# Performance work log

Measured on AMD Instinct MI355X. Metric: run time of the kernel, lower is better.

The kernel has to match this reference:

```python
import jax, jax.numpy as jnp
import numpy as np

N_NODES = 20000   # len(pert2id)
N_EDGES = 400000  # top_20 graph: ~20 edges/node
BATCH   = 4096
IN_DIM  = 64
HID_DIM = 128
OUT_DIM = 64
HEADS   = 2
HEAD_D  = HID_DIM // HEADS  # 64 (also OUT_DIM per head on last layer)


def setup_inputs() -> dict:
    key = jax.random.key(0)
    ks = jax.random.split(key, 24)
    inp = {
        "pert_indices": jax.random.randint(ks[0], (BATCH,), 0, N_NODES),
        "edge_index": jax.random.randint(ks[1], (2, N_EDGES), 0, N_NODES),
        "edge_weight": jax.random.uniform(ks[2], (N_EDGES,), dtype=jnp.float32),
        "emb": jax.random.normal(ks[3], (N_NODES, IN_DIM), dtype=jnp.float32) * 0.02,
    }
    # 4 GATv2 layers: layer0 IN->HEADS*HEAD_D (concat), layers 1,2 HID->HEADS*HEAD_D (concat),
    # layer3 HID->HEADS*OUT_DIM (mean over heads -> OUT_DIM)
    in_dims = [IN_DIM, HID_DIM, HID_DIM, HID_DIM]
    concat = [True, True, True, False]
    k = 4
    for i in range(4):
        d_in = in_dims[i]
        d_head = HEAD_D
        sc = 1.0 / np.sqrt(d_in)
        inp[f"Wl{i}"] = jax.random.normal(ks[k], (d_in, HEADS * d_head), dtype=jnp.float32) * sc; k += 1
        inp[f"Wr{i}"] = jax.random.normal(ks[k], (d_in, HEADS * d_head), dtype=jnp.float32) * sc; k += 1
        inp[f"a{i}"]  = jax.random.normal(ks[k], (HEADS, d_head), dtype=jnp.float32) * (1.0 / np.sqrt(d_head)); k += 1
        out_dim = HEADS * d_head if concat[i] else d_head
        inp[f"b{i}"]  = jnp.zeros((out_dim,), dtype=jnp.float32); k += 1
    return inp


def _gatv2_layer(x, src, dst, ew, Wl, Wr, a, b, concat):
    N = x.shape[0]
    H, D = a.shape
    xl = (x @ Wl).reshape(N, H, D)   # source transform (messages)
    xr = (x @ Wr).reshape(N, H, D)   # target transform
    # GATv2 score: a^T LeakyReLU(Wl x_j + Wr x_i) per edge, per head -> [E, H]
    e = jnp.einsum("ehd,hd->eh", jax.nn.leaky_relu(xl[src] + xr[dst], 0.2), a)
    # segment softmax over incoming edges of each target node
    m = jax.ops.segment_max(e, dst, num_segments=N)
    m = jnp.where(jnp.isfinite(m), m, 0.0)  # isolated nodes
    ex = jnp.exp(e - m[dst])
    s = jax.ops.segment_sum(ex, dst, num_segments=N)
    alpha = ex / (s[dst] + 1e-16)            # [E, H]
    msg = (alpha * ew[:, None])[:, :, None] * xl[src]  # edge-weighted messages [E,H,D]
    out = jax.ops.segment_sum(msg, dst, num_segments=N)  # [N,H,D]
    out = out.reshape(N, H * D) if concat else out.mean(axis=1)
    return out + b


def reference(pert_indices, edge_index, edge_weight, emb,
              Wl0, Wr0, a0, b0, Wl1, Wr1, a1, b1,
              Wl2, Wr2, a2, b2, Wl3, Wr3, a3, b3):
    src, dst = edge_index[0], edge_index[1]
    layers = [(Wl0, Wr0, a0, b0, True), (Wl1, Wr1, a1, b1, True),
              (Wl2, Wr2, a2, b2, True), (Wl3, Wr3, a3, b3, False)]
    x = emb
    for i, (Wl, Wr, a, b, cc) in enumerate(layers):
        x = _gatv2_layer(x, src, dst, edge_weight, Wl, Wr, a, b, cc)
        if i < len(layers) - 1:
            x = jax.nn.elu(x)
    # node_emb[pert_indices]
    return x[pert_indices]
```

## Files before the change

### kernel.cpp

```cpp
#include <hip/hip_runtime.h>
#include <hip/hip_fp16.h>
#include <math.h>

#define N_NODES 20000
#define N_EDGES 400000
#define BATCH   4096
#define MTILES  (N_NODES / 16)
#define XSCALE  1024.0f
#define XINV    (1.0f / 1024.0f)

typedef __attribute__((ext_vector_type(8))) short short8v;
typedef __attribute__((ext_vector_type(4))) float f32x4;

__device__ __forceinline__ void bf16split(float v, short& h, short& l)
{
    unsigned u  = __float_as_uint(v);
    unsigned hu = u & 0xFFFF0000u;
    h = (short)(hu >> 16);
    const float lo = v - __uint_as_float(hu);
    l = (short)(__float_as_uint(lo) >> 16);
}

__global__ __launch_bounds__(256)
void pack_w_all_kernel(const float* __restrict__ Wl0, const float* __restrict__ Wr0,
                       const float* __restrict__ Wl1, const float* __restrict__ Wr1,
                       const float* __restrict__ Wl2, const float* __restrict__ Wr2,
                       const float* __restrict__ Wl3, const float* __restrict__ Wr3,
                       short* __restrict__ wpk)
{
    const int t = blockIdx.x * 256 + threadIdx.x;
    if (t >= 14336) return;
    int layer, base, K;
    const float *Wl, *Wr;
    if (t < 2048)       { layer = 0; base = 0;     K = 64;  Wl = Wl0; Wr = Wr0; }
    else if (t < 6144)  { layer = 1; base = 2048;  K = 128; Wl = Wl1; Wr = Wr1; }
    else if (t < 10240) { layer = 2; base = 6144;  K = 128; Wl = Wl2; Wr = Wr2; }
    else                { layer = 3; base = 10240; K = 128; Wl = Wl3; Wr = Wr3; }
    const int KB   = K / 32;
    const int tt   = t - base;
    const int lane = tt & 63;
    const int kb   = (tt >> 6) % KB;
    const int nt   = tt / (64 * KB);
    const float* W = (nt < 8) ? Wl : Wr;
    const int col  = (nt & 7) * 16 + (lane & 15);
    const int k0   = kb * 32 + (lane >> 4) * 8;
    short8v h, l;
#pragma unroll
    for (int e = 0; e < 8; ++e) {
        short hh, ll; bf16split(W[(size_t)(k0 + e) * 128 + col], hh, ll);
        h[e] = hh; l[e] = ll;
    }
    short* ob = wpk + (size_t)layer * 65536
                    + ((size_t)(nt * KB + kb) * 2) * 512 + lane * 8;
    *(short8v*)ob         = h;
    *(short8v*)(ob + 512) = l;
}

template<int KB, int NWAVES>
__global__ __launch_bounds__(NWAVES * 64)
void mfma_transform_kernel(const float* __restrict__ x,
                           const short* __restrict__ wpk,
                           __half* __restrict__ xlh, float* __restrict__ xr)
{
    constexpr int K  = KB * 32;
    constexpr int KP = K + 4;
    __shared__ float xs[16 * KP];
    const int mtile = blockIdx.x;
    const int wid   = threadIdx.x >> 6;
    const int lane  = threadIdx.x & 63;

    {
        const float4* __restrict__ src = (const float4*)(x + (size_t)mtile * 16 * K);
        for (int idx = threadIdx.x; idx < 16 * K / 4; idx += NWAVES * 64) {
            const int row = idx / (K / 4), c4 = idx % (K / 4);
            *(float4*)(xs + row * KP + c4 * 4) = src[idx];
        }
    }
    __syncthreads();

    short8v ah[KB], al[KB];
    {
        const float* ab = xs + (lane & 15) * KP + (lane >> 4) * 8;
#pragma unroll
        for (int kb = 0; kb < KB; ++kb) {
            const float4 f0 = *(const float4*)(ab + kb * 32);
            const float4 f1 = *(const float4*)(ab + kb * 32 + 4);
            float tmp[8] = {f0.x, f0.y, f0.z, f0.w, f1.x, f1.y, f1.z, f1.w};
#pragma unroll
            for (int e = 0; e < 8; ++e) {
                short hh, ll; bf16split(tmp[e], hh, ll);
                ah[kb][e] = hh; al[kb][e] = ll;
            }
        }
    }

#pragma unroll
    for (int i = 0; i < 4; ++i) {
        const int nt = wid * 4 + i;
        const short* bb = wpk + ((size_t)nt * KB * 2) * 512 + lane * 8;
        f32x4 acc = {0.f, 0.f, 0.f, 0.f};
#pragma unroll
        for (int kb = 0; kb < KB; ++kb) {
            const short8v bh = *(const short8v*)(bb + (size_t)(kb * 2 + 0) * 512);
            const short8v bl = *(const short8v*)(bb + (size_t)(kb * 2 + 1) * 512);
            acc = __builtin_amdgcn_mfma_f32_16x16x32_bf16(ah[kb], bh, acc, 0, 0, 0);
            acc = __builtin_amdgcn_mfma_f32_16x16x32_bf16(ah[kb], bl, acc, 0, 0, 0);
            acc = __builtin_amdgcn_mfma_f32_16x16x32_bf16(al[kb], bh, acc, 0, 0, 0);
        }
        const int colb = (nt & 7) * 16 + (lane & 15);
        const int row0 = mtile * 16 + (lane >> 4) * 4;
        if (nt < 8) {
#pragma unroll
            for (int r = 0; r < 4; ++r)
                xlh[(size_t)(row0 + r) * 128 + colb] = __float2half(acc[r] * XSCALE);
        } else {
#pragma unroll
            for (int r = 0; r < 4; ++r)
                xr[(size_t)(row0 + r) * 128 + colb] = acc[r];
        }
    }
}

template<int K, int G>
__global__ __launch_bounds__(128)
void transform_r_pert_kernel(const float* __restrict__ x,
                             const int* __restrict__ pert,
                             const float* __restrict__ W,
                             float* __restrict__ out)
{
    const int t  = threadIdx.x;
    const int i0 = blockIdx.x * G;

    const float* __restrict__ xrow[G];
#pragma unroll
    for (int g = 0; g < G; ++g)
        xrow[g] = x + (size_t)pert[i0 + g] * K;

    float acc[G];
#pragma unroll
    for (int g = 0; g < G; ++g) acc[g] = 0.f;

    float4 xA[G], xB[G];
    float wA[4], wB[4];

    auto loadc = [&](float4* xs, float* w, int k) {
#pragma unroll
        for (int g = 0; g < G; ++g)
            xs[g] = *(const float4*)(xrow[g] + k);
#pragma unroll
        for (int u = 0; u < 4; ++u) w[u] = W[(k + u) * 128 + t];
    };
    auto fmac = [&](const float4* xs, const float* w) {
#pragma unroll
        for (int g = 0; g < G; ++g) {
            acc[g] = fmaf(xs[g].x, w[0], acc[g]);
            acc[g] = fmaf(xs[g].y, w[1], acc[g]);
            acc[g] = fmaf(xs[g].z, w[2], acc[g]);
            acc[g] = fmaf(xs[g].w, w[3], acc[g]);
        }
    };

    loadc(xA, wA, 0);
    for (int k0 = 0; k0 < K; k0 += 8) {
        if (k0 + 4 < K) loadc(xB, wB, k0 + 4);
        fmac(xA, wA);
        if (k0 + 8 < K) loadc(xA, wA, k0 + 8);
        fmac(xB, wB);
    }

#pragma unroll
    for (int g = 0; g < G; ++g)
        out[(size_t)(i0 + g) * 128 + t] = acc[g];
}

__global__ __launch_bounds__(256)
void zero_kernel(int* __restrict__ p, int n)
{
    const int i = blockIdx.x * blockDim.x + threadIdx.x;
    if (i < n) p[i] = 0;
}

__global__ __launch_bounds__(256)
void count_deg_kernel(const int* __restrict__ dst, int* __restrict__ deg, int E)
{
    const int e = blockIdx.x * blockDim.x + threadIdx.x;
    if (e < E) atomicAdd(&deg[dst[e]], 1);
}

#define CHUNK 20
#define SCAN_PAD (1024 * CHUNK)
__global__ __launch_bounds__(1024)
void scan_kernel(const int* __restrict__ deg, int* __restrict__ off,
                 int* __restrict__ cursor)
{
    __shared__ int xs[SCAN_PAD];
    __shared__ int sums[1024];
    const int t = threadIdx.x;
    for (int i = t; i < SCAN_PAD; i += 1024)
        xs[i] = (i < N_NODES) ? deg[i] : 0;
    __syncthreads();

    const int base = t * CHUNK;
    int local[CHUNK];
    int s = 0;
#pragma unroll
    for (int i = 0; i < CHUNK; ++i) {
        local[i] = s;
        s += xs[base + i];
    }
    sums[t] = s;
    __syncthreads();
    for (int d = 1; d < 1024; d <<= 1) {
        int v = (t >= d) ? sums[t - d] : 0;
        __syncthreads();
        sums[t] += v;
        __syncthreads();
    }
    const int prev = (t == 0) ? 0 : sums[t - 1];
#pragma unroll
    for (int i = 0; i < CHUNK; ++i)
        xs[base + i] = prev + local[i];
    __syncthreads();
    for (int i = t; i < N_NODES; i += 1024) {
        const int o = xs[i];
        off[i] = o;
        cursor[i] = o;
    }
    if (t == 1023) off[N_NODES] = sums[1023];
}

__global__ __launch_bounds__(256)
void scatter_kernel(const int* __restrict__ src, const int* __restrict__ dst,
                    const float* __restrict__ ew, int* __restrict__ cursor,
                    int* __restrict__ ssrc, float* __restrict__ sew, int E)
{
    const int e = blockIdx.x * blockDim.x + threadIdx.x;
    if (e >= E) return;
    const int p = atomicAdd(&cursor[dst[e]], 1);
    ssrc[p] = src[e];
    sew[p]  = ew[e];
}

template<int LAST>
__global__ __launch_bounds__(256)
void gat_node_kernel(const __half* __restrict__ xl, const float* __restrict__ xr,
                     const int* __restrict__ off, const int* __restrict__ ssrc,
                     const float* __restrict__ sew, const float* __restrict__ a,
                     const float* __restrict__ b, float* __restrict__ xout,
                     const int* __restrict__ nodemap, int nnodes)
{
    const int widx = (int)((blockIdx.x * blockDim.x + threadIdx.x) >> 6);
    if (widx >= nnodes) return;
    const int node = LAST ? nodemap[widx] : widx;
    const int xrrow = widx;
    const int lane = threadIdx.x & 63;
    const int q  = lane >> 4;
    const int h  = (lane >> 3) & 1;
    const int j  = lane & 7;
    const int cb = h * 64 + j * 8;

    const float* xrp = xr + (size_t)xrrow * 128 + cb;
    const float4 rA = make_float4(xrp[0] * XSCALE, xrp[1] * XSCALE,
                                  xrp[2] * XSCALE, xrp[3] * XSCALE);
    const float4 rB = make_float4(xrp[4] * XSCALE, xrp[5] * XSCALE,
                                  xrp[6] * XSCALE, xrp[7] * XSCALE);
    const float4 aA = *(const float4*)(a + cb);
    const float4 aB = *(const float4*)(a + cb + 4);

    const int e0 = off[node], e1 = off[node + 1];
    const int nr = (e1 - e0 + 3) >> 2;

    float m = -1e30f, s = 0.f;
    float4 accA = {0,0,0,0}, accB = {0,0,0,0};

    auto ldh8 = [](const __half* p, float4& lo, float4& hi) {
        const uint4 raw = *(const uint4*)p;
        const float2 f0 = __half22float2(*(const __half2*)&raw.x);
        const float2 f1 = __half22float2(*(const __half2*)&raw.y);
        const float2 f2 = __half22float2(*(const __half2*)&raw.z);
        const float2 f3 = __half22float2(*(const __half2*)&raw.w);
        lo = make_float4(f0.x, f0.y, f1.x, f1.y);
        hi = make_float4(f2.x, f2.y, f3.x, f3.y);
    };
    auto lrelu4 = [](float4 v) {
        v.x = fmaxf(v.x, 0.2f * v.x); v.y = fmaxf(v.y, 0.2f * v.y);
        v.z = fmaxf(v.z, 0.2f * v.z); v.w = fmaxf(v.w, 0.2f * v.w);
        return v;
    };
    auto dot4 = [](float4 u, float4 v) {
        return fmaf(u.x, v.x, fmaf(u.y, v.y, fmaf(u.z, v.z, u.w * v.w)));
    };
    auto upd4 = [](float4 acc, float r, float c, float4 xv) {
        acc.x = fmaf(c, xv.x, acc.x * r); acc.y = fmaf(c, xv.y, acc.y * r);
        acc.z = fmaf(c, xv.z, acc.z * r); acc.w = fmaf(c, xv.w, acc.w * r);
        return acc;
    };
    auto lde = [&](int r, float& w, bool& valid, float4& xA, float4& xB) {
        const int ei  = e0 + r * 4 + q;
        valid = ei < e1;
        const int eic = valid ? ei : (e1 - 1);
        const int sn  = ssrc[eic];
        w = valid ? sew[eic] : 0.f;
        ldh8(xl + (size_t)sn * 128 + cb, xA, xB);
    };

    float w_c; bool v_c; float4 xA_c, xB_c;
    if (nr > 0) lde(0, w_c, v_c, xA_c, xB_c);

    for (int r = 0; r < nr; ++r) {
        float w_n; bool v_n; float4 xA_n, xB_n;
        if (r + 1 < nr) lde(r + 1, w_n, v_n, xA_n, xB_n);

        const float4 vA = lrelu4(make_float4(xA_c.x + rA.x, xA_c.y + rA.y,
                                             xA_c.z + rA.z, xA_c.w + rA.w));
        const float4 vB = lrelu4(make_float4(xB_c.x + rB.x, xB_c.y + rB.y,
                                             xB_c.z + rB.z, xB_c.w + rB.w));
        float p = dot4(vA, aA) + dot4(vB, aB);
        p += __shfl_xor(p, 1, 64);
        p += __shfl_xor(p, 2, 64);
        p += __shfl_xor(p, 4, 64);
        p = v_c ? p * XINV : -1e30f;

        const float d   = p - m;
        const float t   = __expf(-fabsf(d));
        const bool  pos = d > 0.f;
        const float rr  = pos ? t : 1.f;
        const float ex  = pos ? 1.f : t;
        m = pos ? p : m;
        const float c = ex * w_c;
        s = s * rr + ex;
        accA = upd4(accA, rr, c, xA_c);
        accB = upd4(accB, rr, c, xB_c);

        w_c = w_n; v_c = v_n; xA_c = xA_n; xB_c = xB_n;
    }

    float mg = fmaxf(m, __shfl_xor(m, 16, 64));
    mg = fmaxf(mg, __shfl_xor(mg, 32, 64));
    const float rq = __expf(m - mg);
    float sq = s * rq;
    sq += __shfl_xor(sq, 16, 64);
    sq += __shfl_xor(sq, 32, 64);
    auto redsum2 = [](float v) {
        v += __shfl_xor(v, 16, 64);
        return v + __shfl_xor(v, 32, 64);
    };
    accA.x = redsum2(accA.x * rq); accA.y = redsum2(accA.y * rq);
    accA.z = redsum2(accA.z * rq); accA.w = redsum2(accA.w * rq);
    accB.x = redsum2(accB.x * rq); accB.y = redsum2(accB.y * rq);
    accB.z = redsum2(accB.z * rq); accB.w = redsum2(accB.w * rq);
    const float inv = XINV / (sq + 1e-16f);

    if (!LAST) {
        if (q == 0) {
            const float4 bA = *(const float4*)(b + cb);
            const float4 bB = *(const float4*)(b + cb + 4);
            float4 oA, oB;
            oA.x = accA.x * inv + bA.x; oA.x = oA.x > 0.f ? oA.x : expm1f(oA.x);
            oA.y = accA.y * inv + bA.y; oA.y = oA.y > 0.f ? oA.y : expm1f(oA.y);
            oA.z = accA.z * inv + bA.z; oA.z = oA.z > 0.f ? oA.z : expm1f(oA.z);
            oA.w = accA.w * inv + bA.w; oA.w = oA.w > 0.f ? oA.w : expm1f(oA.w);
            oB.x = accB.x * inv + bB.x; oB.x = oB.x > 0.f ? oB.x : expm1f(oB.x);
            oB.y = accB.y * inv + bB.y; oB.y = oB.y > 0.f ? oB.y : expm1f(oB.y);
            oB.z = accB.z * inv + bB.z; oB.z = oB.z > 0.f ? oB.z : expm1f(oB.z);
            oB.w = accB.w * inv + bB.w; oB.w = oB.w > 0.f ? oB.w : expm1f(oB.w);
            float* op = xout + (size_t)node * 128;
            *(float4*)(op + cb)     = oA;
            *(float4*)(op + cb + 4) = oB;
        }
    } else {
        float oA[4] = {accA.x * inv, accA.y * inv, accA.z * inv, accA.w * inv};
        float oB[4] = {accB.x * inv, accB.y * inv, accB.z * inv, accB.w * inv};
        float pA[4], pB[4];
#pragma unroll
        for (int k = 0; k < 4; ++k) {
            pA[k] = __shfl_xor(oA[k], 8, 64);
            pB[k] = __shfl_xor(oB[k], 8, 64);
        }
        if (q == 0 && h == 0) {
            const float4 bA = *(const float4*)(b + j * 8);
            const float4 bB = *(const float4*)(b + j * 8 + 4);
            float* op = xout + (size_t)widx * 64 + j * 8;
            op[0] = 0.5f * (oA[0] + pA[0]) + bA.x;
            op[1] = 0.5f * (oA[1] + pA[1]) + bA.y;
            op[2] = 0.5f * (oA[2] + pA[2]) + bA.z;
            op[3] = 0.5f * (oA[3] + pA[3]) + bA.w;
            op[4] = 0.5f * (oB[0] + pB[0]) + bB.x;
            op[5] = 0.5f * (oB[1] + pB[1]) + bB.y;
            op[6] = 0.5f * (oB[2] + pB[2]) + bB.z;
            op[7] = 0.5f * (oB[3] + pB[3]) + bB.w;
        }
    }
}

extern "C" void kernel_launch(void* const* d_in, const int* in_sizes, int n_in,
                              void* d_out, int out_size, void* d_ws, size_t ws_size,
                              hipStream_t stream)
{
    const int*   pert = (const int*)d_in[0];
    const int*   eidx = (const int*)d_in[1];
    const float* ew   = (const float*)d_in[2];
    const float* emb  = (const float*)d_in[3];
    const float* Wl[4] = {(const float*)d_in[4],  (const float*)d_in[8],
                          (const float*)d_in[12], (const float*)d_in[16]};
    const float* Wr[4] = {(const float*)d_in[5],  (const float*)d_in[9],
                          (const float*)d_in[13], (const float*)d_in[17]};
    const float* av[4] = {(const float*)d_in[6],  (const float*)d_in[10],
                          (const float*)d_in[14], (const float*)d_in[18]};
    const float* bv[4] = {(const float*)d_in[7],  (const float*)d_in[11],
                          (const float*)d_in[15], (const float*)d_in[19]};

    const int N = N_NODES, E = N_EDGES;
    const int* srcp = eidx;
    const int* dstp = eidx + E;

    float*  ws   = (float*)d_ws;
    float*  xbuf = ws;
    __half* xlh  = (__half*)(xbuf + (size_t)N * 128);
    float*  xr   = (float*)(xlh + (size_t)N * 128);
    short*  wpk  = (short*)(xr + (size_t)N * 128);
    int*    deg  = (int*)(wpk + 4 * 65536);
    int*    off  = deg + N;
    int*    cur  = off + N + 1;
    int*    ssrc = cur + N;
    float*  sew  = (float*)(ssrc + E);

    zero_kernel<<<(N + 255) / 256, 256, 0, stream>>>(deg, N);
    count_deg_kernel<<<(E + 255) / 256, 256, 0, stream>>>(dstp, deg, E);
    scan_kernel<<<1, 1024, 0, stream>>>(deg, off, cur);
    scatter_kernel<<<(E + 255) / 256, 256, 0, stream>>>(srcp, dstp, ew, cur,
                                                        ssrc, sew, E);

    pack_w_all_kernel<<<56, 256, 0, stream>>>(Wl[0], Wr[0], Wl[1], Wr[1],
                                              Wl[2], Wr[2], Wl[3], Wr[3], wpk);

    mfma_transform_kernel<2, 4><<<MTILES, 256, 0, stream>>>(emb, wpk, xlh, xr);
    gat_node_kernel<0><<<(N * 64 + 255) / 256, 256, 0, stream>>>(
        xlh, xr, off, ssrc, sew, av[0], bv[0], xbuf, nullptr, N);

    for (int layer = 1; layer < 3; ++layer) {
        mfma_transform_kernel<4, 4><<<MTILES, 256, 0, stream>>>(
            xbuf, wpk + layer * 65536, xlh, xr);
        gat_node_kernel<0><<<(N * 64 + 255) / 256, 256, 0, stream>>>(
            xlh, xr, off, ssrc, sew, av[layer], bv[layer], xbuf, nullptr, N);
    }

    mfma_transform_kernel<4, 2><<<MTILES, 128, 0, stream>>>(
        xbuf, wpk + 3 * 65536, xlh, xr);
    transform_r_pert_kernel<128, 8><<<BATCH / 8, 128, 0, stream>>>(
        xbuf, pert, Wr[3], xr);
    gat_node_kernel<1><<<(BATCH * 64 + 255) / 256, 256, 0, stream>>>(
        xlh, xr, off, ssrc, sew, av[3], bv[3], (float*)d_out, pert, BATCH);
}
```

Before: 237.9 us.

## Merge prep kernels, fuse layer-3 transforms, add lazy-rescale online softmax

After: 234.6 us. About the same (-1.4%).

```diff
diff --git a/kernel.cpp b/kernel.cpp
--- a/kernel.cpp
+++ b/kernel.cpp
@@ -22,22 +22,25 @@
 }
 
 __global__ __launch_bounds__(256)
-void pack_w_all_kernel(const float* __restrict__ Wl0, const float* __restrict__ Wr0,
-                       const float* __restrict__ Wl1, const float* __restrict__ Wr1,
-                       const float* __restrict__ Wl2, const float* __restrict__ Wr2,
-                       const float* __restrict__ Wl3, const float* __restrict__ Wr3,
-                       short* __restrict__ wpk)
+void prep_kernel(int* __restrict__ deg,
+                 const float* __restrict__ Wl0, const float* __restrict__ Wr0,
+                 const float* __restrict__ Wl1, const float* __restrict__ Wr1,
+                 const float* __restrict__ Wl2, const float* __restrict__ Wr2,
+                 const float* __restrict__ Wl3, const float* __restrict__ Wr3,
+                 short* __restrict__ wpk)
 {
     const int t = blockIdx.x * 256 + threadIdx.x;
-    if (t >= 14336) return;
+    if (t < N_NODES) { deg[t] = 0; return; }
+    const int tp = t - N_NODES;
+    if (tp >= 14336) return;
     int layer, base, K;
     const float *Wl, *Wr;
-    if (t < 2048)       { layer = 0; base = 0;     K = 64;  Wl = Wl0; Wr = Wr0; }
-    else if (t < 6144)  { layer = 1; base = 2048;  K = 128; Wl = Wl1; Wr = Wr1; }
-    else if (t < 10240) { layer = 2; base = 6144;  K = 128; Wl = Wl2; Wr = Wr2; }
-    else                { layer = 3; base = 10240; K = 128; Wl = Wl3; Wr = Wr3; }
+    if (tp < 2048)       { layer = 0; base = 0;     K = 64;  Wl = Wl0; Wr = Wr0; }
+    else if (tp < 6144)  { layer = 1; base = 2048;  K = 128; Wl = Wl1; Wr = Wr1; }
+    else if (tp < 10240) { layer = 2; base = 6144;  K = 128; Wl = Wl2; Wr = Wr2; }
+    else                 { layer = 3; base = 10240; K = 128; Wl = Wl3; Wr = Wr3; }
     const int KB   = K / 32;
-    const int tt   = t - base;
+    const int tt   = tp - base;
     const int lane = tt & 63;
     const int kb   = (tt >> 6) % KB;
     const int nt   = tt / (64 * KB);
@@ -121,63 +124,108 @@
     }
 }
 
-template<int K, int G>
 __global__ __launch_bounds__(128)
-void transform_r_pert_kernel(const float* __restrict__ x,
-                             const int* __restrict__ pert,
-                             const float* __restrict__ W,
-                             float* __restrict__ out)
-{
-    const int t  = threadIdx.x;
-    const int i0 = blockIdx.x * G;
-
-    const float* __restrict__ xrow[G];
-#pragma unroll
-    for (int g = 0; g < G; ++g)
-        xrow[g] = x + (size_t)pert[i0 + g] * K;
-
-    float acc[G];
-#pragma unroll
-    for (int g = 0; g < G; ++g) acc[g] = 0.f;
-
-    float4 xA[G], xB[G];
-    float wA[4], wB[4];
-
-    auto loadc = [&](float4* xs, float* w, int k) {
+void l3_fused_kernel(const float* __restrict__ x, const short* __restrict__ wpk,
+                     __half* __restrict__ xlh,
+                     const int* __restrict__ pert, const float* __restrict__ Wr3,
+                     float* __restrict__ xr)
+{
+    constexpr int K  = 128;
+    constexpr int KP = K + 4;
+    __shared__ float xs[16 * KP];
+
+    if (blockIdx.x < MTILES) {
+        const int mtile = blockIdx.x;
+        const int wid   = threadIdx.x >> 6;
+        const int lane  = threadIdx.x & 63;
+        {
+            const float4* __restrict__ src = (const float4*)(x + (size_t)mtile * 16 * K);
+            for (int idx = threadIdx.x; idx < 16 * K / 4; idx += 128) {
+                const int row = idx / (K / 4), c4 = idx % (K / 4);
+                *(float4*)(xs + row * KP + c4 * 4) = src[idx];
+            }
+        }
+        __syncthreads();
+
+        short8v ah[4], al[4];
+        {
+            const float* ab = xs + (lane & 15) * KP + (lane >> 4) * 8;
+#pragma unroll
+            for (int kb = 0; kb < 4; ++kb) {
+                const float4 f0 = *(const float4*)(ab + kb * 32);
+                const float4 f1 = *(const float4*)(ab + kb * 32 + 4);
+                float tmp[8] = {f0.x, f0.y, f0.z, f0.w, f1.x, f1.y, f1.z, f1.w};
+#pragma unroll
+                for (int e = 0; e < 8; ++e) {
+                    short hh, ll; bf16split(tmp[e], hh, ll);
+                    ah[kb][e] = hh; al[kb][e] = ll;
+                }
+            }
+        }
+#pragma unroll
+        for (int i = 0; i < 4; ++i) {
+            const int nt = wid * 4 + i;
+            const short* bb = wpk + ((size_t)nt * 4 * 2) * 512 + lane * 8;
+            f32x4 acc = {0.f, 0.f, 0.f, 0.f};
+#pragma unroll
+            for (int kb = 0; kb < 4; ++kb) {
+                const short8v bh = *(const short8v*)(bb + (size_t)(kb * 2 + 0) * 512);
+                const short8v bl = *(const short8v*)(bb + (size_t)(kb * 2 + 1) * 512);
+                acc = __builtin_amdgcn_mfma_f32_16x16x32_bf16(ah[kb], bh, acc, 0, 0, 0);
+                acc = __builtin_amdgcn_mfma_f32_16x16x32_bf16(ah[kb], bl, acc, 0, 0, 0);
+                acc = __builtin_amdgcn_mfma_f32_16x16x32_bf16(al[kb], bh, acc, 0, 0, 0);
+            }
+            const int colb = (nt & 7) * 16 + (lane & 15);
+            const int row0 = mtile * 16 + (lane >> 4) * 4;
+#pragma unroll
+            for (int r = 0; r < 4; ++r)
+                xlh[(size_t)(row0 + r) * 128 + colb] = __float2half(acc[r] * XSCALE);
+        }
+    } else {
+        constexpr int G = 8;
+        const int t  = threadIdx.x;
+        const int i0 = (blockIdx.x - MTILES) * G;
+
+        const float* __restrict__ xrow[G];
 #pragma unroll
         for (int g = 0; g < G; ++g)
-            xs[g] = *(const float4*)(xrow[g] + k);
-#pragma unroll
-        for (int u = 0; u < 4; ++u) w[u] = W[(k + u) * 128 + t];
-    };
-    auto fmac = [&](const float4* xs, const float* w) {
-#pragma unroll
-        for (int g = 0; g < G; ++g) {
-            acc[g] = fmaf(xs[g].x, w[0], acc[g]);
-            acc[g] = fmaf(xs[g].y, w[1], acc[g]);
-            acc[g] = fmaf(xs[g].z, w[2], acc[g]);
-            acc[g] = fmaf(xs[g].w, w[3], acc[g]);
-        }
-    };
-
-    loadc(xA, wA, 0);
-    for (int k0 = 0; k0 < K; k0 += 8) {
-        if (k0 + 4 < K) loadc(xB, wB, k0 + 4);
-        fmac(xA, wA);
-        if (k0 + 8 < K) loadc(xA, wA, k0 + 8);
-        fmac(xB, wB);
-    }
-
-#pragma unroll
-    for (int g = 0; g < G; ++g)
-        out[(size_t)(i0 + g) * 128 + t] = acc[g];
-}
-
-__global__ __launch_bounds__(256)
-void zero_kernel(int* __restrict__ p, int n)
-{
-    const int i = blockIdx.x * blockDim.x + threadIdx.x;
-    if (i < n) p[i] = 0;
+            xrow[g] = x + (size_t)pert[i0 + g] * K;
+
+        float acc[G];
+#pragma unroll
+        for (int g = 0; g < G; ++g) acc[g] = 0.f;
+
+        float4 xA[G], xB[G];
+        float wA[4], wB[4];
+
+        auto loadc = [&](float4* xv, float* w, int k) {
+#pragma unroll
+            for (int g = 0; g < G; ++g)
+                xv[g] = *(const float4*)(xrow[g] + k);
+#pragma unroll
+            for (int u = 0; u < 4; ++u) w[u] = Wr3[(k + u) * 128 + t];
+        };
+        auto fmac = [&](const float4* xv, const float* w) {
+#pragma unroll
+            for (int g = 0; g < G; ++g) {
+                acc[g] = fmaf(xv[g].x, w[0], acc[g]);
+                acc[g] = fmaf(xv[g].y, w[1], acc[g]);
+                acc[g] = fmaf(xv[g].z, w[2], acc[g]);
+                acc[g] = fmaf(xv[g].w, w[3], acc[g]);
+            }
+        };
+
+        loadc(xA, wA, 0);
+        for (int k0 = 0; k0 < K; k0 += 8) {
+            if (k0 + 4 < K) loadc(xB, wB, k0 + 4);
+            fmac(xA, wA);
+            if (k0 + 8 < K) loadc(xA, wA, k0 + 8);
+            fmac(xB, wB);
+        }
+#pragma unroll
+        for (int g = 0; g < G; ++g)
+            xr[(size_t)(i0 + g) * 128 + t] = acc[g];
+    }
 }
 
 __global__ __launch_bounds__(256)
@@ -295,6 +343,11 @@
         acc.z = fmaf(c, xv.z, acc.z * r); acc.w = fmaf(c, xv.w, acc.w * r);
         return acc;
     };
+    auto fma4 = [](float4 acc, float c, float4 xv) {
+        acc.x = fmaf(c, xv.x, acc.x); acc.y = fmaf(c, xv.y, acc.y);
+        acc.z = fmaf(c, xv.z, acc.z); acc.w = fmaf(c, xv.w, acc.w);
+        return acc;
+    };
     auto lde = [&](int r, float& w, bool& valid, float4& xA, float4& xB) {
         const int ei  = e0 + r * 4 + q;
         valid = ei < e1;
@@ -321,16 +374,24 @@
         p += __shfl_xor(p, 4, 64);
         p = v_c ? p * XINV : -1e30f;
 
-        const float d   = p - m;
-        const float t   = __expf(-fabsf(d));
-        const bool  pos = d > 0.f;
-        const float rr  = pos ? t : 1.f;
-        const float ex  = pos ? 1.f : t;
-        m = pos ? p : m;
-        const float c = ex * w_c;
-        s = s * rr + ex;
-        accA = upd4(accA, rr, c, xA_c);
-        accB = upd4(accB, rr, c, xB_c);
+        const float d = p - m;
+        if (__any(d > 8.f)) {
+            const float t   = __expf(-fabsf(d));
+            const bool  pos = d > 0.f;
+            const float rr  = pos ? t : 1.f;
+            const float ex  = pos ? 1.f : t;
+            m = pos ? p : m;
+            const float c = ex * w_c;
+            s = s * rr + ex;
+            accA = upd4(accA, rr, c, xA_c);
+            accB = upd4(accB, rr, c, xB_c);
+        } else {
+            const float ex = __expf(d);
+            const float c  = ex * w_c;
+            s += ex;
+            accA = fma4(accA, c, xA_c);
+            accB = fma4(accB, c, xB_c);
+        }
 
         w_c = w_n; v_c = v_n; xA_c = xA_n; xB_c = xB_n;
     }
@@ -425,14 +486,12 @@
     int*    ssrc = cur + N;
     float*  sew  = (float*)(ssrc + E);
 
-    zero_kernel<<<(N + 255) / 256, 256, 0, stream>>>(deg, N);
+    prep_kernel<<<(N + 14336 + 255) / 256, 256, 0, stream>>>(
+        deg, Wl[0], Wr[0], Wl[1], Wr[1], Wl[2], Wr[2], Wl[3], Wr[3], wpk);
     count_deg_kernel<<<(E + 255) / 256, 256, 0, stream>>>(dstp, deg, E);
     scan_kernel<<<1, 1024, 0, stream>>>(deg, off, cur);
     scatter_kernel<<<(E + 255) / 256, 256, 0, stream>>>(srcp, dstp, ew, cur,
                                                         ssrc, sew, E);
-
-    pack_w_all_kernel<<<56, 256, 0, stream>>>(Wl[0], Wr[0], Wl[1], Wr[1],
-                                              Wl[2], Wr[2], Wl[3], Wr[3], wpk);
 
     mfma_transform_kernel<2, 4><<<MTILES, 256, 0, stream>>>(emb, wpk, xlh, xr);
     gat_node_kernel<0><<<(N * 64 + 255) / 256, 256, 0, stream>>>(
@@ -445,10 +504,8 @@
             xlh, xr, off, ssrc, sew, av[layer], bv[layer], xbuf, nullptr, N);
     }
 
-    mfma_transform_kernel<4, 2><<<MTILES, 128, 0, stream>>>(
-        xbuf, wpk + 3 * 65536, xlh, xr);
-    transform_r_pert_kernel<128, 8><<<BATCH / 8, 128, 0, stream>>>(
-        xbuf, pert, Wr[3], xr);
+    l3_fused_kernel<<<MTILES + BATCH / 8, 128, 0, stream>>>(
+        xbuf, wpk + 3 * 65536, xlh, pert, Wr[3], xr);
     gat_node_kernel<1><<<(BATCH * 64 + 255) / 256, 256, 0, stream>>>(
         xlh, xr, off, ssrc, sew, av[3], bv[3], (float*)d_out, pert, BATCH);
 }
```
